# Kernel tuning notes

Measured on AMD Instinct MI355X. Metric: run time of the kernel, lower is better.

The kernel has to match this reference:

```python
import jax, jax.numpy as jnp
import numpy as np

B, N, C, K = 64, 32768, 2, 10   # batch, num predictions, num classes, padded GT slots (build_target default N=10)
VL = 1.0e6                      # 'very_large' sentinel from torch code
EPS = 1e-08
W_LOC = W_CLASS = W_CONF = 1.0


def setup_inputs() -> dict:
    key = jax.random.key(0)
    k1, k2, k3, k4, k5, k6, k7 = jax.random.split(key, 7)
    p_start = jax.random.normal(k1, (B, N), dtype=jnp.float32)
    p_end = jax.random.normal(k2, (B, N), dtype=jnp.float32)
    p_class_logits = jax.random.normal(k3, (B, N, C), dtype=jnp.float32)
    p_conf_logits = jax.random.normal(k4, (B, N), dtype=jnp.float32)
    # GT intervals in [0,1] (compared against sigmoid(pred)); class channel in {0,1}
    fs = jax.random.uniform(k5, (B, K), dtype=jnp.float32)
    fe = jnp.clip(fs + 0.2 * jax.random.uniform(k6, (B, K), dtype=jnp.float32), 0.0, 1.0)
    cls = jax.random.randint(k7, (B, K), 0, C).astype(jnp.float32)
    gt_boxes = jnp.stack([fs, fe, cls], axis=-1)  # (B, K, 3)
    return {'p_start': p_start, 'p_end': p_end, 'p_class_logits': p_class_logits,
            'p_conf_logits': p_conf_logits, 'gt_boxes': gt_boxes}


def _build_target(gt_boxes):
    fs, fe, cls = gt_boxes[..., 0], gt_boxes[..., 1], gt_boxes[..., 2]
    presence = (~(jnp.isnan(fs) | jnp.isnan(fe) | jnp.isnan(cls))).astype(jnp.float32)
    fs = jnp.nan_to_num(fs)
    fe = jnp.nan_to_num(fe)
    cls = jnp.nan_to_num(cls)
    onehot = jax.nn.one_hot(jnp.clip(cls.astype(jnp.int32), 0, C - 1), C, dtype=jnp.float32)
    return fs, fe, onehot, presence


def _match_and_losses(cost, ps, pe, pcl, pconf, fs, fe, onehot):
    # cost: (K, N); greedy one-to-one argmin matching with row/col masking.
    Kp, Np = cost.shape

    def step(c, _):
        flat = c.reshape(-1)
        idx = jnp.argmin(flat)
        val = flat[idx]
        row, col = idx // Np, idx % Np
        valid = val < VL / 2
        c = c.at[row, :].set(VL).at[:, col].set(VL)
        return c, (row, col, valid)

    _, (rows, cols, valids) = jax.lax.scan(step, jax.lax.stop_gradient(cost), None, length=Kp)
    vm = valids.astype(jnp.float32)  # (K,)

    sel_s = jax.nn.sigmoid(ps[cols])
    sel_e = jax.nn.sigmoid(pe[cols])
    gs, ge = fs[rows], fe[rows]
    loc = (sel_s - gs) ** 2 + (sel_e - ge) ** 2

    logits = pcl[cols]          # (K, C)
    y = onehot[rows]            # (K, C)
    bce = (y * jax.nn.softplus(-logits) + (1.0 - y) * jax.nn.softplus(logits)).sum(-1)

    # IoU target is computed from .item() values in torch -> constant (no grad)
    ss, se = jax.lax.stop_gradient(sel_s), jax.lax.stop_gradient(sel_e)
    gss, gse = jax.lax.stop_gradient(gs), jax.lax.stop_gradient(ge)
    a1, b1 = jnp.minimum(ss, se), jnp.maximum(ss, se)
    a2, b2 = jnp.minimum(gss, gse), jnp.maximum(gss, gse)
    inter = jnp.maximum(0.0, jnp.minimum(b1, b2) - jnp.maximum(a1, a2))
    union = jnp.maximum(EPS, jnp.maximum(b1, b2) - jnp.minimum(a1, a2))
    iou = inter / union
    conf = (jax.nn.sigmoid(pconf[cols]) - iou) ** 2

    return (loc * vm).sum(), (bce * vm).sum(), (conf * vm).sum(), vm.sum()


def reference(p_start, p_end, p_class_logits, p_conf_logits, gt_boxes):
    fs, fe, onehot, presence = _build_target(gt_boxes)  # (B,K), (B,K), (B,K,C), (B,K)
    ps_sig = jax.nn.sigmoid(p_start)
    pe_sig = jax.nn.sigmoid(p_end)
    # loc MSE cost: (B, K, N)
    loc = (ps_sig[:, None, :] - fs[:, :, None]) ** 2 + (pe_sig[:, None, :] - fe[:, :, None]) ** 2
    # class L2 cost without materializing (B,K,N,C): |a-b|^2 = |a|^2 - 2 a.b + |b|^2
    sc = jax.nn.sigmoid(p_class_logits)  # (B, N, C)
    class_l2 = ((sc ** 2).sum(-1)[:, None, :]
                - 2.0 * jnp.einsum('bnc,bkc->bkn', sc, onehot)
                + (onehot ** 2).sum(-1)[:, :, None])
    cost = loc + class_l2
    # invalid (absent) GT rows get sentinel cost so greedy skips them
    cost = jnp.where(presence[:, :, None] > 0, cost, VL)

    loc_s, cls_s, conf_s, m = jax.vmap(_match_and_losses)(
        cost, p_start, p_end, p_class_logits, p_conf_logits, fs, fe, onehot)

    total_m = m.sum()
    denom = total_m + EPS
    total = (W_LOC * loc_s.sum() + W_CLASS * cls_s.sum() + W_CONF * conf_s.sum()) / denom
    return jnp.where(total_m > 0, total, 0.0)
```

## Files before the change

kernel.cpp:

```cpp
#include <hip/hip_runtime.h>
#include <cfloat>
#include <cmath>

#define BB 64
#define NN 32768
#define CC 2
#define KK 10
#define S_SL 32
#define SLICE (NN / S_SL)
#define TPM 256
#define VLARGE 1.0e6
#define KEY_MAX 0xFFFFFFFFFFFFFFFFull
#define BND_MARGIN 1.0e-3

__device__ __forceinline__ double dsig(float x) { return 1.0 / (1.0 + exp(-(double)x)); }
__device__ __forceinline__ double dsoftplus(double x) {
    return fmax(x, 0.0) + log1p(exp(-fabs(x)));
}
__device__ __forceinline__ unsigned long long packkey(float v, int c) {
    return ((unsigned long long)__float_as_uint(v) << 32) | (unsigned int)c;
}
__device__ __forceinline__ void merge2(unsigned long long& a1, unsigned long long& a2,
                                       unsigned long long b1, unsigned long long b2) {
    unsigned long long lo = a1 < b1 ? a1 : b1;
    unsigned long long hi = a1 < b1 ? b1 : a1;
    unsigned long long mb = a2 < b2 ? a2 : b2;
    a2 = hi < mb ? hi : mb;
    a1 = lo;
}
__device__ __forceinline__ void colterms(float sraw, float eraw, float q0raw, float q1raw,
                                         float& s, float& e, float& u0, float& u1) {
    s = __fdividef(1.0f, 1.0f + __expf(-sraw));
    e = __fdividef(1.0f, 1.0f + __expf(-eraw));
    const float q0 = __fdividef(1.0f, 1.0f + __expf(-q0raw));
    const float q1 = __fdividef(1.0f, 1.0f + __expf(-q1raw));
    const float se2 = fmaf(s, s, e * e);
    const float t0 = q0 - 1.0f, t1 = q1 - 1.0f;
    u0 = se2 + fmaf(t0, t0, q1 * q1);
    u1 = se2 + fmaf(t1, t1, q0 * q0);
}
__device__ __forceinline__ float rowcost(float s, float e, float u0, float u1,
                                         float m0, float m1, float ckv, int cls, int pres) {
    float c = fmaf(m0, s, fmaf(m1, e, ((cls == 0) ? u0 : u1) + ckv));
    c = fmaxf(c, 0.0f);
    return pres ? c : (float)VLARGE;
}
__device__ __forceinline__ double eval64(const float* ps, const float* pe, const float* pc,
                                         double fs, double fe, int cls, int pres, int col) {
    if (!pres) return VLARGE;
    const double s  = dsig(ps[col]);
    const double e  = dsig(pe[col]);
    const double q0 = dsig(pc[2 * col]);
    const double q1 = dsig(pc[2 * col + 1]);
    const double d0 = s - fs, d1 = e - fe;
    const double sc = (cls == 0) ? q0 : q1;
    return d0 * d0 + d1 * d1 + (q0 * q0 + q1 * q1 - 2.0 * sc + 1.0);
}

__global__ __launch_bounds__(64)
void scan_kernel(const float* __restrict__ p_start, const float* __restrict__ p_end,
                 const float* __restrict__ p_cls, const float* __restrict__ gt,
                 ulonglong2* __restrict__ cand) {
    const int sl = blockIdx.x, b = blockIdx.y, j = threadIdx.x;
    const float2* ps2 = (const float2*)(p_start + (size_t)b * NN);
    const float2* pe2 = (const float2*)(p_end   + (size_t)b * NN);
    const float4* pc4 = (const float4*)(p_cls   + (size_t)b * NN * CC);

    float m0[KK], m1[KK], ck[KK]; int rcl[KK], rpres[KK];
    #pragma unroll
    for (int k = 0; k < KK; k++) {
        float f0 = gt[((size_t)b * KK + k) * 3 + 0];
        float f1 = gt[((size_t)b * KK + k) * 3 + 1];
        float f2 = gt[((size_t)b * KK + k) * 3 + 2];
        int pres = !(isnan(f0) || isnan(f1) || isnan(f2));
        if (isnan(f0)) f0 = 0.0f;
        if (isnan(f1)) f1 = 0.0f;
        if (isnan(f2)) f2 = 0.0f;
        int ci = (int)f2; ci = ci < 0 ? 0 : (ci > CC - 1 ? CC - 1 : ci);
        m0[k] = -2.0f * f0; m1[k] = -2.0f * f1;
        ck[k] = fmaf(f0, f0, f1 * f1);
        rcl[k] = ci; rpres[k] = pres;
    }

    float v1[KK], v2[KK]; int c1[KK], c2[KK];
    #pragma unroll
    for (int k = 0; k < KK; k++) { v1[k] = FLT_MAX; v2[k] = FLT_MAX; c1[k] = 0x7fffffff; c2[k] = 0x7fffffff; }

    const int base = sl * SLICE;
    #pragma unroll
    for (int it = 0; it < SLICE / 128; it++) {
        const int pidx = (base >> 1) + it * 64 + j;
        const float2 sv = ps2[pidx];
        const float2 ev = pe2[pidx];
        const float4 cv = pc4[pidx];
        #pragma unroll
        for (int h = 0; h < 2; h++) {
            const int n = 2 * pidx + h;
            float s, e, u0, u1;
            colterms(h ? sv.y : sv.x, h ? ev.y : ev.x,
                     h ? cv.z : cv.x, h ? cv.w : cv.y, s, e, u0, u1);
            #pragma unroll
            for (int k = 0; k < KK; k++) {
                const float cost = rowcost(s, e, u0, u1, m0[k], m1[k], ck[k], rcl[k], rpres[k]);
                const bool lt1 = cost < v1[k], lt2 = cost < v2[k];
                v2[k] = lt2 ? (lt1 ? v1[k] : cost) : v2[k];
                c2[k] = lt2 ? (lt1 ? c1[k] : n)    : c2[k];
                v1[k] = lt1 ? cost : v1[k];
                c1[k] = lt1 ? n    : c1[k];
            }
        }
    }

    unsigned long long k1[KK], k2[KK];
    #pragma unroll
    for (int k = 0; k < KK; k++) { k1[k] = packkey(v1[k], c1[k]); k2[k] = packkey(v2[k], c2[k]); }
    #pragma unroll
    for (int off = 1; off < 64; off <<= 1) {
        #pragma unroll
        for (int k = 0; k < KK; k++) {
            unsigned long long o1 = __shfl_xor(k1[k], off, 64);
            unsigned long long o2 = __shfl_xor(k2[k], off, 64);
            merge2(k1[k], k2[k], o1, o2);
        }
    }
    if (j == 0) {
        #pragma unroll
        for (int k = 0; k < KK; k++) {
            ulonglong2 pk; pk.x = k1[k]; pk.y = k2[k];
            cand[((size_t)b * S_SL + sl) * KK + k] = pk;
        }
    }
}

__global__ __launch_bounds__(TPM)
void match_kernel(const float* __restrict__ p_start, const float* __restrict__ p_end,
                  const float* __restrict__ p_cls, const float* __restrict__ p_conf,
                  const float* __restrict__ gt, const ulonglong2* __restrict__ cand,
                  double* __restrict__ partials) {
    const int b = blockIdx.x, tid = threadIdx.x;
    const int j = tid & 63, wv = tid >> 6;
    const float* ps  = p_start + (size_t)b * NN;
    const float* pe  = p_end   + (size_t)b * NN;
    const float* pc  = p_cls   + (size_t)b * NN * CC;
    const float* pcf = p_conf  + (size_t)b * NN;

    __shared__ double l_cost[KK][64];
    __shared__ int    l_col[KK][64];
    __shared__ double l_bnd[KK][S_SL];
    __shared__ double gfs[KK], gfe[KK];
    __shared__ int    gcls[KK], gpres[KK];

    if (tid < KK) {
        float f0 = gt[((size_t)b * KK + tid) * 3 + 0];
        float f1 = gt[((size_t)b * KK + tid) * 3 + 1];
        float f2 = gt[((size_t)b * KK + tid) * 3 + 2];
        int pres = !(isnan(f0) || isnan(f1) || isnan(f2));
        if (isnan(f0)) f0 = 0.0f;
        if (isnan(f1)) f1 = 0.0f;
        if (isnan(f2)) f2 = 0.0f;
        int ci = (int)f2; ci = ci < 0 ? 0 : (ci > CC - 1 ? CC - 1 : ci);
        gfs[tid] = (double)f0; gfe[tid] = (double)f1;
        gcls[tid] = ci; gpres[tid] = pres;
    }
    __syncthreads();

    for (int idx = tid; idx < KK * 64; idx += TPM) {
        const int r = idx >> 6, jj = idx & 63, sl = jj >> 1;
        ulonglong2 pk = cand[((size_t)b * S_SL + sl) * KK + r];
        const unsigned long long key = (jj & 1) ? pk.y : pk.x;
        int c = (int)(unsigned int)(key & 0xffffffffull);
        if (c < 0 || c >= NN) c = 0;
        l_cost[r][jj] = eval64(ps, pe, pc, gfs[r], gfe[r], gcls[r], gpres[r], c);
        l_col[r][jj]  = c;
        if (jj & 1)
            l_bnd[r][sl] = (double)__uint_as_float((unsigned int)(key >> 32)) - BND_MARGIN;
    }
    __syncthreads();
    if (wv != 0) return;

    const int s_my = j >> 1;
    double val[KK]; int col[KK]; double bnd[KK];
    #pragma unroll
    for (int r = 0; r < KK; r++) {
        val[r] = l_cost[r][j]; col[r] = l_col[r][j]; bnd[r] = l_bnd[r][s_my];
    }

    unsigned act = (1u << KK) - 1;
    int cons[KK], prow[KK], pcolv[KK], pvalid[KK];
    #pragma unroll
    for (int r = 0; r < KK; r++) cons[r] = -1;

    for (int step = 0; step < KK; step++) {
        double bv = DBL_MAX; int brow = 0x7fffffff, bcol = 0x7fffffff;
        for (int guard = 0; guard < 64; guard++) {
            double lv = DBL_MAX; int lr = 0x7fffffff, lc = 0x7fffffff;
            #pragma unroll
            for (int r = 0; r < KK; r++) {
                if (!((act >> r) & 1)) continue;
                const int pcold = __shfl(col[r], j ^ 1, 64);
                const bool mine  = (col[r] >= 0);
                const bool bound = !mine && (pcold < 0) && ((j & 1) == 0);
                const double v = mine ? val[r] : (bound ? bnd[r] : DBL_MAX);
                const int    c = mine ? col[r] : (bound ? (-2 - s_my) : 0x7fffffff);
                if (v < lv || (v == lv && (r < lr || (r == lr && c < lc)))) {
                    lv = v; lr = r; lc = c;
                }
            }
            #pragma unroll
            for (int off = 1; off < 64; off <<= 1) {
                const double ov = __shfl_xor(lv, off, 64);
                const int   orr = __shfl_xor(lr, off, 64);
                const int   oc  = __shfl_xor(lc, off, 64);
                if (ov < lv || (ov == lv && (orr < lr || (orr == lr && oc < lc)))) {
                    lv = ov; lr = orr; lc = oc;
                }
            }
            bv = lv; brow = lr; bcol = lc;
            if (bcol >= 0 || bv == DBL_MAX) break;

            const int ss = -2 - bcol;
            const float ffs = (float)gfs[brow], ffe = (float)gfe[brow];
            const int   cb  = gcls[brow], pb = gpres[brow];
            const float m0b = -2.0f * ffs, m1b = -2.0f * ffe;
            const float ckb = fmaf(ffs, ffs, ffe * ffe);
            unsigned long long r1 = KEY_MAX, r2 = KEY_MAX;
            const int cbase = ss * SLICE;
            for (int t = j; t < SLICE; t += 64) {
                const int n = cbase + t;
                bool used = false;
                #pragma unroll
                for (int u = 0; u < KK; u++) used |= (cons[u] == n);
                float s, e, u0, u1;
                colterms(ps[n], pe[n], pc[2 * n], pc[2 * n + 1], s, e, u0, u1);
                const float cst = rowcost(s, e, u0, u1, m0b, m1b, ckb, cb, pb);
                const unsigned long long kk = used ? KEY_MAX : packkey(cst, n);
                if (kk < r2) { if (kk < r1) { r2 = r1; r1 = kk; } else { r2 = kk; } }
            }
            #pragma unroll
            for (int off = 1; off < 64; off <<= 1) {
                const unsigned long long o1 = __shfl_xor(r1, off, 64);
                const unsigned long long o2 = __shfl_xor(r2, off, 64);
                merge2(r1, r2, o1, o2);
            }
            int cA = (int)(unsigned int)(r1 & 0xffffffffull);
            int cB = (int)(unsigned int)(r2 & 0xffffffffull);
            if (cA < 0 || cA >= NN) cA = 0;
            if (cB < 0 || cB >= NN) cB = 0;
            const double vA = (r1 == KEY_MAX) ? DBL_MAX
                : eval64(ps, pe, pc, gfs[brow], gfe[brow], cb, pb, cA);
            const double vB = (r2 == KEY_MAX) ? DBL_MAX
                : eval64(ps, pe, pc, gfs[brow], gfe[brow], cb, pb, cB);
            const double nb = (r2 == KEY_MAX) ? DBL_MAX
                : (double)__uint_as_float((unsigned int)(r2 >> 32)) - BND_MARGIN;
            #pragma unroll
            for (int r = 0; r < KK; r++) {
                if (r != brow) continue;
                if (j == 2 * ss)     { val[r] = vA; col[r] = (r1 == KEY_MAX) ? -1 : cA; }
                if (j == 2 * ss + 1) { val[r] = vB; col[r] = (r2 == KEY_MAX) ? -1 : cB; }
                if (s_my == ss) bnd[r] = nb;
            }
        }

        prow[step]   = brow;
        pcolv[step]  = bcol;
        pvalid[step] = (bv < VLARGE * 0.5) && (bcol >= 0) && (brow < KK);
        cons[step]   = (bcol >= 0) ? bcol : -1;
        if (brow < KK) act &= ~(1u << brow);
        else break;

        if (bcol >= 0) {
            #pragma unroll
            for (int r = 0; r < KK; r++)
                if (col[r] == bcol) col[r] = -1;
        }
    }

    double loss = 0.0, m = 0.0;
    if (j < KK && pvalid[j]) {
        const int r = prow[j], cidx = pcolv[j];
        const double ss = dsig(ps[cidx]);
        const double se = dsig(pe[cidx]);
        const double gs = gfs[r], ge = gfe[r];
        const double d0 = ss - gs, d1 = se - ge;
        double acc = d0 * d0 + d1 * d1;

        const double l0 = (double)pc[2 * cidx];
        const double l1 = (double)pc[2 * cidx + 1];
        const double y0 = (gcls[r] == 0) ? 1.0 : 0.0;
        const double y1 = 1.0 - y0;
        acc += y0 * dsoftplus(-l0) + (1.0 - y0) * dsoftplus(l0)
             + y1 * dsoftplus(-l1) + (1.0 - y1) * dsoftplus(l1);

        const double a1 = fmin(ss, se), b1 = fmax(ss, se);
        const double a2 = fmin(gs, ge), b2 = fmax(gs, ge);
        const double inter = fmax(0.0, fmin(b1, b2) - fmax(a1, a2));
        const double uni   = fmax(1e-8, fmax(b1, b2) - fmin(a1, a2));
        const double iou   = inter / uni;
        const double dcf   = dsig(pcf[cidx]) - iou;
        acc += dcf * dcf;
        loss = acc; m = 1.0;
    }
    #pragma unroll
    for (int off = 1; off < 64; off <<= 1) {
        loss += __shfl_xor(loss, off, 64);
        m    += __shfl_xor(m, off, 64);
    }
    if (j == 0) { partials[b * 2 + 0] = loss; partials[b * 2 + 1] = m; }
}

__global__ void finalize_kernel(const double* __restrict__ partials,
                                float* __restrict__ out, int out_size) {
    const int t = threadIdx.x;
    for (int i = t; i < out_size; i += 64) out[i] = 0.0f;
    double s = partials[t * 2 + 0];
    double m = partials[t * 2 + 1];
    for (int off = 32; off > 0; off >>= 1) {
        s += __shfl_down(s, off, 64);
        m += __shfl_down(m, off, 64);
    }
    if (t == 0) {
        const double total = s / (m + 1e-8);
        out[0] = (float)(m > 0.0 ? total : 0.0);
    }
}

extern "C" void kernel_launch(void* const* d_in, const int* in_sizes, int n_in,
                              void* d_out, int out_size, void* d_ws, size_t ws_size,
                              hipStream_t stream) {
    const float* p_start = (const float*)d_in[0];
    const float* p_end   = (const float*)d_in[1];
    const float* p_cls   = (const float*)d_in[2];
    const float* p_conf  = (const float*)d_in[3];
    const float* gt      = (const float*)d_in[4];

    ulonglong2* cand     = (ulonglong2*)d_ws;
    double*     partials = (double*)((char*)d_ws + (size_t)BB * S_SL * KK * sizeof(ulonglong2));

    scan_kernel<<<dim3(S_SL, BB), 64, 0, stream>>>(p_start, p_end, p_cls, gt, cand);
    match_kernel<<<BB, TPM, 0, stream>>>(p_start, p_end, p_cls, p_conf, gt, cand, partials);
    finalize_kernel<<<1, 64, 0, stream>>>(partials, (float*)d_out, out_size);
}
```

Before: 148.1 us.

## Widen scan blocks to four waves and fold finalize into match via atomic ticket

The scan kernel now uses 256 threads per slice instead of 64, so each wave handles a quarter of the slice and the four wave results are merged through shared memory. This cuts each thread's serial loop from eight iterations to two and raises parallelism. The separate finalize launch is removed: the last match block, picked by an atomic counter, does the final reduction, which saves one kernel launch but adds a memset and threadfences.

```diff
diff --git a/kernel.cpp b/kernel.cpp
--- a/kernel.cpp
+++ b/kernel.cpp
@@ -8,6 +8,7 @@
 #define KK 10
 #define S_SL 32
 #define SLICE (NN / S_SL)
+#define TPS 256
 #define TPM 256
 #define VLARGE 1.0e6
 #define KEY_MAX 0xFFFFFFFFFFFFFFFFull
@@ -57,11 +58,12 @@
     return d0 * d0 + d1 * d1 + (q0 * q0 + q1 * q1 - 2.0 * sc + 1.0);
 }
 
-__global__ __launch_bounds__(64)
+__global__ __launch_bounds__(TPS)
 void scan_kernel(const float* __restrict__ p_start, const float* __restrict__ p_end,
                  const float* __restrict__ p_cls, const float* __restrict__ gt,
                  ulonglong2* __restrict__ cand) {
-    const int sl = blockIdx.x, b = blockIdx.y, j = threadIdx.x;
+    const int sl = blockIdx.x, b = blockIdx.y;
+    const int tid = threadIdx.x, wv = tid >> 6, lane = tid & 63;
     const float2* ps2 = (const float2*)(p_start + (size_t)b * NN);
     const float2* pe2 = (const float2*)(p_end   + (size_t)b * NN);
     const float4* pc4 = (const float4*)(p_cls   + (size_t)b * NN * CC);
@@ -86,10 +88,10 @@
     #pragma unroll
     for (int k = 0; k < KK; k++) { v1[k] = FLT_MAX; v2[k] = FLT_MAX; c1[k] = 0x7fffffff; c2[k] = 0x7fffffff; }
 
-    const int base = sl * SLICE;
-    #pragma unroll
-    for (int it = 0; it < SLICE / 128; it++) {
-        const int pidx = (base >> 1) + it * 64 + j;
+    const int base2 = sl * (SLICE / 2) + wv * 128;
+    #pragma unroll
+    for (int it = 0; it < 2; it++) {
+        const int pidx = base2 + it * 64 + lane;
         const float2 sv = ps2[pidx];
         const float2 ev = pe2[pidx];
         const float4 cv = pc4[pidx];
@@ -123,12 +125,18 @@
             merge2(k1[k], k2[k], o1, o2);
         }
     }
-    if (j == 0) {
-        #pragma unroll
-        for (int k = 0; k < KK; k++) {
-            ulonglong2 pk; pk.x = k1[k]; pk.y = k2[k];
-            cand[((size_t)b * S_SL + sl) * KK + k] = pk;
-        }
+    __shared__ unsigned long long s1[4][KK], s2[4][KK];
+    if (lane == 0) {
+        #pragma unroll
+        for (int k = 0; k < KK; k++) { s1[wv][k] = k1[k]; s2[wv][k] = k2[k]; }
+    }
+    __syncthreads();
+    if (tid < KK) {
+        unsigned long long a1 = s1[0][tid], a2 = s2[0][tid];
+        #pragma unroll
+        for (int w = 1; w < 4; w++) merge2(a1, a2, s1[w][tid], s2[w][tid]);
+        ulonglong2 pk; pk.x = a1; pk.y = a2;
+        cand[((size_t)b * S_SL + sl) * KK + tid] = pk;
     }
 }
 
@@ -136,7 +144,8 @@
 void match_kernel(const float* __restrict__ p_start, const float* __restrict__ p_end,
                   const float* __restrict__ p_cls, const float* __restrict__ p_conf,
                   const float* __restrict__ gt, const ulonglong2* __restrict__ cand,
-                  double* __restrict__ partials) {
+                  double* __restrict__ partials, unsigned int* __restrict__ counter,
+                  float* __restrict__ out, int out_size) {
     const int b = blockIdx.x, tid = threadIdx.x;
     const int j = tid & 63, wv = tid >> 6;
     const float* ps  = p_start + (size_t)b * NN;
@@ -188,7 +197,7 @@
     unsigned act = (1u << KK) - 1;
     int cons[KK], prow[KK], pcolv[KK], pvalid[KK];
     #pragma unroll
-    for (int r = 0; r < KK; r++) cons[r] = -1;
+    for (int r = 0; r < KK; r++) { cons[r] = -1; pvalid[r] = 0; prow[r] = 0; pcolv[r] = 0; }
 
     for (int step = 0; step < KK; step++) {
         double bv = DBL_MAX; int brow = 0x7fffffff, bcol = 0x7fffffff;
@@ -306,21 +315,25 @@
         m    += __shfl_xor(m, off, 64);
     }
     if (j == 0) { partials[b * 2 + 0] = loss; partials[b * 2 + 1] = m; }
-}
-
-__global__ void finalize_kernel(const double* __restrict__ partials,
-                                float* __restrict__ out, int out_size) {
-    const int t = threadIdx.x;
-    for (int i = t; i < out_size; i += 64) out[i] = 0.0f;
-    double s = partials[t * 2 + 0];
-    double m = partials[t * 2 + 1];
-    for (int off = 32; off > 0; off >>= 1) {
-        s += __shfl_down(s, off, 64);
-        m += __shfl_down(m, off, 64);
-    }
-    if (t == 0) {
-        const double total = s / (m + 1e-8);
-        out[0] = (float)(m > 0.0 ? total : 0.0);
+
+    __threadfence();
+    int ticket = 0;
+    if (j == 0) ticket = (int)atomicAdd(counter, 1u);
+    ticket = __shfl(ticket, 0, 64);
+    if (ticket == BB - 1) {
+        __threadfence();
+        for (int i = j; i < out_size; i += 64) out[i] = 0.0f;
+        double s = partials[j * 2 + 0];
+        double mm = partials[j * 2 + 1];
+        #pragma unroll
+        for (int off = 1; off < 64; off <<= 1) {
+            s  += __shfl_xor(s, off, 64);
+            mm += __shfl_xor(mm, off, 64);
+        }
+        if (j == 0) {
+            const double total = s / (mm + 1e-8);
+            out[0] = (float)(mm > 0.0 ? total : 0.0);
+        }
     }
 }
 
@@ -333,10 +346,14 @@
     const float* p_conf  = (const float*)d_in[3];
     const float* gt      = (const float*)d_in[4];
 
-    ulonglong2* cand     = (ulonglong2*)d_ws;
-    double*     partials = (double*)((char*)d_ws + (size_t)BB * S_SL * KK * sizeof(ulonglong2));
-
-    scan_kernel<<<dim3(S_SL, BB), 64, 0, stream>>>(p_start, p_end, p_cls, gt, cand);
-    match_kernel<<<BB, TPM, 0, stream>>>(p_start, p_end, p_cls, p_conf, gt, cand, partials);
-    finalize_kernel<<<1, 64, 0, stream>>>(partials, (float*)d_out, out_size);
-}
+    const size_t cand_bytes = (size_t)BB * S_SL * KK * sizeof(ulonglong2);
+    const size_t part_bytes = (size_t)BB * 2 * sizeof(double);
+    ulonglong2*   cand     = (ulonglong2*)d_ws;
+    double*       partials = (double*)((char*)d_ws + cand_bytes);
+    unsigned int* counter  = (unsigned int*)((char*)d_ws + cand_bytes + part_bytes);
+
+    hipMemsetAsync(counter, 0, sizeof(unsigned int), stream);
+    scan_kernel<<<dim3(S_SL, BB), TPS, 0, stream>>>(p_start, p_end, p_cls, gt, cand);
+    match_kernel<<<BB, TPM, 0, stream>>>(p_start, p_end, p_cls, p_conf, gt, cand,
+                                         partials, counter, (float*)d_out, out_size);
+}
```

New measurement: 165.0 us. 1.11x slower.
